# Kernel tuning notes

Hardware: AMD Instinct MI355X
Metric: run time of the kernel (lower is better)

## Reference

```python
import jax, jax.numpy as jnp
import numpy as np


def setup_inputs() -> dict:
    key = jax.random.key(0)
    k1, k2 = jax.random.split(key)
    B, C, H, W = 4, 64, 256, 512
    l_fmap = jax.random.normal(k1, (B, C, H, W), dtype=jnp.float32)
    r_fmap = jax.random.normal(k2, (B, C, H, W), dtype=jnp.float32)
    return {"l_fmap": l_fmap, "r_fmap": r_fmap, "max_disp": 48}


def reference(l_fmap, r_fmap, max_disp):
    # l_fmap, r_fmap: [B, C, H, W]
    w = l_fmap.shape[-1]
    # zero-pad right fmap along width by max_disp on both sides
    r_pad = jnp.pad(r_fmap, ((0, 0), (0, 0), (0, 0), (max_disp, max_disp)))
    planes = []
    for d in range(-max_disp, max_disp + 1):  # fixed small loop over 2*max_disp+1 disparities
        begin = max_disp - d
        # channel-mean of elementwise correlation at shift d -> [B, H, W]
        planes.append(jnp.mean(l_fmap * r_pad[:, :, :, begin:begin + w], axis=1))
    # cost volume: [B, 2*max_disp+1, H, W]
    return jnp.stack(planes, axis=1)
```

## Files before the change

### kernel.cpp

```cpp
#include <hip/hip_runtime.h>


#define B_  4
#define C_  64
#define H_  256
#define W_  512
#define ND  97
#define NWT 32
#define HW  (H_ * W_)
#define PAD 513
#define CH0 49

typedef __attribute__((ext_vector_type(8))) short  short8;
typedef __attribute__((ext_vector_type(4))) float  floatx4;

__device__ __forceinline__ unsigned f2bf(float f) {
    unsigned u = __builtin_bit_cast(unsigned, f);
    return (u + 0x7FFFu + ((u >> 16) & 1u)) >> 16;
}

union SM {
    struct {
        short l[W_ * C_];
        short r[W_ * C_];
    } st;
    float out_s[CH0 * PAD];
};

__global__ __launch_bounds__(1024, 4) void cost_volume_kernel(
    const float* __restrict__ L, const float* __restrict__ R,
    float* __restrict__ out)
{
    __shared__ SM sm;
    const int tid = threadIdx.x;
    const int h   = blockIdx.x;
    const int b   = blockIdx.y;
    const size_t in_base = (((size_t)b * C_) * H_ + h) * (size_t)W_;

    {
        const int wl = tid & 511;
        const int ch = tid >> 9;
        const int m  = wl & 15, wq = wl >> 4;
        const float* lp = L + in_base + wl;
        const float* rp = R + in_base + wl;
        #pragma unroll
        for (int i = 0; i < 4; ++i) {
            const int cc = ch + 2 * i;
            unsigned dl[4], dr[4];
            #pragma unroll
            for (int jj = 0; jj < 4; ++jj) {
                float l0 = lp[(size_t)(cc * 8 + 2 * jj)     * HW] * 0.015625f;
                float l1 = lp[(size_t)(cc * 8 + 2 * jj + 1) * HW] * 0.015625f;
                float r0 = rp[(size_t)(cc * 8 + 2 * jj)     * HW];
                float r1 = rp[(size_t)(cc * 8 + 2 * jj + 1) * HW];
                dl[jj] = f2bf(l0) | (f2bf(l1) << 16);
                dr[jj] = f2bf(r0) | (f2bf(r1) << 16);
            }
            const int chunk = (wq * 8 + cc) * 16 + m;
            *((uint4*)&sm.st.l[chunk * 8]) = make_uint4(dl[0], dl[1], dl[2], dl[3]);
            *((uint4*)&sm.st.r[chunk * 8]) = make_uint4(dr[0], dr[1], dr[2], dr[3]);
        }
    }
    __syncthreads();

    const int lane = tid & 63;
    const int wv   = tid >> 6;
    const int q    = lane >> 4, m16 = lane & 15;
    const short8* lv = (const short8*)sm.st.l;
    const short8* rv = (const short8*)sm.st.r;

    floatx4 acc[2][7];
    #pragma unroll
    for (int half = 0; half < 2; ++half) {
        const int wt = wv + 16 * half;
        const short8 a0 = lv[(wt * 8 +     q) * 16 + m16];
        const short8 a1 = lv[(wt * 8 + 4 + q) * 16 + m16];
        #pragma unroll
        for (int t = 0; t < 7; ++t) {
            floatx4 c = {0.f, 0.f, 0.f, 0.f};
            const int ut = wt + t - 3;
            if ((unsigned)ut < (unsigned)NWT) {
                const short8 b0 = rv[(ut * 8 +     q) * 16 + m16];
                const short8 b1 = rv[(ut * 8 + 4 + q) * 16 + m16];
                c = __builtin_amdgcn_mfma_f32_16x16x32_bf16(a0, b0, c, 0, 0, 0);
                c = __builtin_amdgcn_mfma_f32_16x16x32_bf16(a1, b1, c, 0, 0, 0);
            }
            acc[half][t] = c;
        }
    }

    float* ob = out + (((size_t)b * ND) * H_ + h) * (size_t)W_;
    int lo = 0;
    #pragma unroll
    for (int ck = 0; ck < 2; ++ck) {
        const int cnt = ck ? (ND - CH0) : CH0;
        __syncthreads();
        #pragma unroll
        for (int half = 0; half < 2; ++half) {
            const int wt = wv + 16 * half;
            #pragma unroll
            for (int t = 0; t < 7; ++t) {
                #pragma unroll
                for (int r = 0; r < 4; ++r) {
                    const int ml    = q * 4 + r;
                    const int d_idx = ml - m16 + 96 - 16 * t;
                    const int drel  = d_idx - lo;
                    if ((unsigned)drel < (unsigned)cnt)
                        sm.out_s[drel * PAD + wt * 16 + ml] = acc[half][t][r];
                }
            }
        }
        __syncthreads();
        for (int i = tid; i < cnt * W_; i += 1024) {
            const int pr = i >> 9, w = i & 511;
            ob[(size_t)(lo + pr) * HW + w] = sm.out_s[pr * PAD + w];
        }
        lo += CH0;
    }
}

extern "C" void kernel_launch(void* const* d_in, const int* in_sizes, int n_in,
                              void* d_out, int out_size, void* d_ws, size_t ws_size,
                              hipStream_t stream) {
    const float* L = (const float*)d_in[0];
    const float* R = (const float*)d_in[1];
    float* out = (float*)d_out;
    (void)in_sizes; (void)n_in; (void)d_ws; (void)ws_size; (void)out_size;
    dim3 grid(H_, B_);
    hipLaunchKernelGGL(cost_volume_kernel, grid, dim3(1024), 0, stream, L, R, out);
}
```

Baseline: 382.2 us.

## Split each row across two blocks with halo loading of right feature map

Each block now handles half a row (256 columns) with 512 threads instead of a full row with 1024 threads, doubling the grid. The right feature map tile is loaded with a 48-column halo on each side, zero-filled at image borders, so the boundary check in the MFMA loop goes away. The intent is smaller blocks and less shared memory per block, which should raise occupancy and improve load balance. The cost is redundant reads of the halo columns of R.

After: 394.2 us. 1.03x slower.

```diff
diff --git a/kernel.cpp b/kernel.cpp
--- a/kernel.cpp
+++ b/kernel.cpp
@@ -6,10 +6,12 @@
 #define H_  256
 #define W_  512
 #define ND  97
-#define NWT 32
 #define HW  (H_ * W_)
-#define PAD 513
-#define CH0 49
+
+#define WBLK 256
+#define RCOL 352
+#define PADH 257
+#define CH0  49
 
 typedef __attribute__((ext_vector_type(8))) short  short8;
 typedef __attribute__((ext_vector_type(4))) float  floatx4;
@@ -21,28 +23,30 @@
 
 union SM {
     struct {
-        short l[W_ * C_];
-        short r[W_ * C_];
+        short l[WBLK * C_];
+        short r[RCOL * C_];
     } st;
-    float out_s[CH0 * PAD];
+    float out_s[CH0 * PADH];
 };
 
-__global__ __launch_bounds__(1024, 4) void cost_volume_kernel(
+__global__ __launch_bounds__(512, 4) void cost_volume_kernel(
     const float* __restrict__ L, const float* __restrict__ R,
     float* __restrict__ out)
 {
     __shared__ SM sm;
-    const int tid = threadIdx.x;
-    const int h   = blockIdx.x;
-    const int b   = blockIdx.y;
+    const int tid  = threadIdx.x;
+    const int half = blockIdx.x;
+    const int h    = blockIdx.y;
+    const int b    = blockIdx.z;
+    const int w0   = half << 8;
     const size_t in_base = (((size_t)b * C_) * H_ + h) * (size_t)W_;
 
     {
-        const int wl = tid & 511;
-        const int ch = tid >> 9;
+        const int wl = tid & 255;
+        const int ch = tid >> 8;
         const int m  = wl & 15, wq = wl >> 4;
-        const float* lp = L + in_base + wl;
-        const float* rp = R + in_base + wl;
+        const float* lp = L + in_base + w0 + wl;
+        const float* rp = R + in_base + w0 + wl;
         #pragma unroll
         for (int i = 0; i < 4; ++i) {
             const int cc = ch + 2 * i;
@@ -56,9 +60,34 @@
                 dl[jj] = f2bf(l0) | (f2bf(l1) << 16);
                 dr[jj] = f2bf(r0) | (f2bf(r1) << 16);
             }
-            const int chunk = (wq * 8 + cc) * 16 + m;
-            *((uint4*)&sm.st.l[chunk * 8]) = make_uint4(dl[0], dl[1], dl[2], dl[3]);
-            *((uint4*)&sm.st.r[chunk * 8]) = make_uint4(dr[0], dr[1], dr[2], dr[3]);
+            const int lchunk = ( wq      * 8 + cc) * 16 + m;
+            const int rchunk = ((wq + 3) * 8 + cc) * 16 + m;
+            *((uint4*)&sm.st.l[lchunk * 8]) = make_uint4(dl[0], dl[1], dl[2], dl[3]);
+            *((uint4*)&sm.st.r[rchunk * 8]) = make_uint4(dr[0], dr[1], dr[2], dr[3]);
+        }
+    }
+    if (tid < 192) {
+        const int ch = tid & 1;
+        const int hl = tid >> 1;
+        const int ul = (hl < 48) ? hl : hl + 256;
+        const int u  = w0 - 48 + ul;
+        const bool valid = (unsigned)u < (unsigned)W_;
+        const int m = ul & 15, uq = ul >> 4;
+        const float* rp = R + in_base + (valid ? u : 0);
+        #pragma unroll
+        for (int i = 0; i < 4; ++i) {
+            const int cc = ch + 2 * i;
+            unsigned dr[4];
+            #pragma unroll
+            for (int jj = 0; jj < 4; ++jj) {
+                float r0 = rp[(size_t)(cc * 8 + 2 * jj)     * HW];
+                float r1 = rp[(size_t)(cc * 8 + 2 * jj + 1) * HW];
+                r0 = valid ? r0 : 0.f;
+                r1 = valid ? r1 : 0.f;
+                dr[jj] = f2bf(r0) | (f2bf(r1) << 16);
+            }
+            const int rchunk = (uq * 8 + cc) * 16 + m;
+            *((uint4*)&sm.st.r[rchunk * 8]) = make_uint4(dr[0], dr[1], dr[2], dr[3]);
         }
     }
     __syncthreads();
@@ -71,33 +100,31 @@
 
     floatx4 acc[2][7];
     #pragma unroll
-    for (int half = 0; half < 2; ++half) {
-        const int wt = wv + 16 * half;
-        const short8 a0 = lv[(wt * 8 +     q) * 16 + m16];
-        const short8 a1 = lv[(wt * 8 + 4 + q) * 16 + m16];
+    for (int hf = 0; hf < 2; ++hf) {
+        const int lt = wv + 8 * hf;
+        const short8 a0 = lv[(lt * 8 +     q) * 16 + m16];
+        const short8 a1 = lv[(lt * 8 + 4 + q) * 16 + m16];
         #pragma unroll
         for (int t = 0; t < 7; ++t) {
+            const int ut = lt + t;
             floatx4 c = {0.f, 0.f, 0.f, 0.f};
-            const int ut = wt + t - 3;
-            if ((unsigned)ut < (unsigned)NWT) {
-                const short8 b0 = rv[(ut * 8 +     q) * 16 + m16];
-                const short8 b1 = rv[(ut * 8 + 4 + q) * 16 + m16];
-                c = __builtin_amdgcn_mfma_f32_16x16x32_bf16(a0, b0, c, 0, 0, 0);
-                c = __builtin_amdgcn_mfma_f32_16x16x32_bf16(a1, b1, c, 0, 0, 0);
-            }
-            acc[half][t] = c;
+            const short8 b0 = rv[(ut * 8 +     q) * 16 + m16];
+            const short8 b1 = rv[(ut * 8 + 4 + q) * 16 + m16];
+            c = __builtin_amdgcn_mfma_f32_16x16x32_bf16(a0, b0, c, 0, 0, 0);
+            c = __builtin_amdgcn_mfma_f32_16x16x32_bf16(a1, b1, c, 0, 0, 0);
+            acc[hf][t] = c;
         }
     }
 
-    float* ob = out + (((size_t)b * ND) * H_ + h) * (size_t)W_;
+    float* ob = out + (((size_t)b * ND) * H_ + h) * (size_t)W_ + w0;
     int lo = 0;
     #pragma unroll
     for (int ck = 0; ck < 2; ++ck) {
         const int cnt = ck ? (ND - CH0) : CH0;
         __syncthreads();
         #pragma unroll
-        for (int half = 0; half < 2; ++half) {
-            const int wt = wv + 16 * half;
+        for (int hf = 0; hf < 2; ++hf) {
+            const int lt = wv + 8 * hf;
             #pragma unroll
             for (int t = 0; t < 7; ++t) {
                 #pragma unroll
@@ -106,14 +133,14 @@
                     const int d_idx = ml - m16 + 96 - 16 * t;
                     const int drel  = d_idx - lo;
                     if ((unsigned)drel < (unsigned)cnt)
-                        sm.out_s[drel * PAD + wt * 16 + ml] = acc[half][t][r];
+                        sm.out_s[drel * PADH + lt * 16 + ml] = acc[hf][t][r];
                 }
             }
         }
         __syncthreads();
-        for (int i = tid; i < cnt * W_; i += 1024) {
-            const int pr = i >> 9, w = i & 511;
-            ob[(size_t)(lo + pr) * HW + w] = sm.out_s[pr * PAD + w];
+        for (int i = tid; i < cnt * WBLK; i += 512) {
+            const int pr = i >> 8, w = i & 255;
+            ob[(size_t)(lo + pr) * HW + w] = sm.out_s[pr * PADH + w];
         }
         lo += CH0;
     }
@@ -126,6 +153,6 @@
     const float* R = (const float*)d_in[1];
     float* out = (float*)d_out;
     (void)in_sizes; (void)n_in; (void)d_ws; (void)ws_size; (void)out_size;
-    dim3 grid(H_, B_);
-    hipLaunchKernelGGL(cost_volume_kernel, grid, dim3(1024), 0, stream, L, R, out);
+    dim3 grid(2, H_, B_);
+    hipLaunchKernelGGL(cost_volume_kernel, grid, dim3(512), 0, stream, L, R, out);
 }
```
